# Kernel optimization log

Measured on AMD Instinct MI355X. Metric: run time of the kernel, lower is better.

The kernel has to match this reference:

```python
import jax, jax.numpy as jnp
import numpy as np

N = 100000     # nodes
H = 128        # hidden_channels == in_channels
OUT = 64       # out_channels
L = 3          # num_layers=4 -> num_layers-1 Layer modules
E = 1_600_000  # unique undirected edges (avg degree 16)
BN_EPS = 1e-5


def _make_edges():
    # Unique undirected edges, no self-loops -> dense symmetric adjacency in the
    # original module is exactly this edge set symmetrized.
    rng = np.random.default_rng(0)
    i = rng.integers(0, N, 1_700_000)
    j = rng.integers(0, N, 1_700_000)
    m = i != j
    i, j = i[m], j[m]
    lo, hi = np.minimum(i, j), np.maximum(i, j)
    pairs = np.unique(lo.astype(np.int64) * N + hi)[:E]
    lo = (pairs // N).astype(np.int32)
    hi = (pairs % N).astype(np.int32)
    src = jnp.asarray(np.concatenate([lo, hi]))  # [2E] directed
    dst = jnp.asarray(np.concatenate([hi, lo]))
    return src, dst


def setup_inputs() -> dict:
    key = jax.random.key(0)
    ks = jax.random.split(key, 24)
    nrm = lambda k, s: (jax.random.normal(k, s, dtype=jnp.float32) * 0.05)
    src, dst = _make_edges()
    return {
        "x": jax.random.normal(ks[0], (N, H), dtype=jnp.float32),
        "src": src,
        "dst": dst,
        # per-Layer MLP(in=H, hidden=H, out=H): Linear->ReLU->Linear, stacked over L
        "layer_W1": nrm(ks[1], (L, H, H)),
        "layer_b1": nrm(ks[2], (L, H)),
        "layer_W2": nrm(ks[3], (L, H, H)),
        "layer_b2": nrm(ks[4], (L, H)),
        # BatchNorm1d (eval mode: running stats)
        "bn_gamma": 1.0 + nrm(ks[5], (L, H)),
        "bn_beta": nrm(ks[6], (L, H)),
        "bn_mean": nrm(ks[7], (L, H)),
        "bn_var": jax.random.uniform(ks[8], (L, H), jnp.float32, 0.5, 1.5),
        # single shared GRUCell(H, H)
        "gru_Wih": nrm(ks[9], (3 * H, H)),
        "gru_Whh": nrm(ks[10], (3 * H, H)),
        "gru_bih": nrm(ks[11], (3 * H,)),
        "gru_bhh": nrm(ks[12], (3 * H,)),
        # mlp_last: MLP(H, H, OUT)
        "last_W1": nrm(ks[13], (H, H)),
        "last_b1": nrm(ks[14], (H,)),
        "last_W2": nrm(ks[15], (OUT, H)),
        "last_b2": nrm(ks[16], (OUT,)),
    }


def reference(x, src, dst, layer_W1, layer_b1, layer_W2, layer_b2,
              bn_gamma, bn_beta, bn_mean, bn_var,
              gru_Wih, gru_Whh, gru_bih, gru_bhh,
              last_W1, last_b1, last_W2, last_b2):
    n = x.shape[0]
    deg = jax.ops.segment_sum(jnp.ones(src.shape[0], x.dtype), dst, num_segments=n)
    inv_deg = (1.0 / jnp.maximum(deg, 1.0))[:, None]  # isolated nodes -> 0 agg
    h = jnp.zeros((n, H), x.dtype)
    for l in range(L):
        agg = jax.ops.segment_sum(x[src], dst, num_segments=n) * inv_deg  # mean over neighbors
        c = x + agg
        c = jnp.maximum(c @ layer_W1[l].T + layer_b1[l], 0.0) @ layer_W2[l].T + layer_b2[l]
        c = bn_gamma[l] * (c - bn_mean[l]) * jax.lax.rsqrt(bn_var[l] + BN_EPS) + bn_beta[l]
        # F.dropout(training=False) is identity
        gi = c @ gru_Wih.T + gru_bih  # [n, 3H]
        gh = h @ gru_Whh.T + gru_bhh
        r = jax.nn.sigmoid(gi[:, :H] + gh[:, :H])
        z = jax.nn.sigmoid(gi[:, H:2 * H] + gh[:, H:2 * H])
        nst = jnp.tanh(gi[:, 2 * H:] + r * gh[:, 2 * H:])
        h = (1.0 - z) * nst + z * h
        x = h
    return jnp.maximum(x @ last_W1.T + last_b1, 0.0) @ last_W2.T + last_b2
```

## Files before the change

### kernel.cpp

```cpp
#include <hip/hip_runtime.h>
#include <hip/hip_bf16.h>
#include <stdint.h>

typedef __bf16 bf16;
typedef __bf16 bf16x8 __attribute__((ext_vector_type(8)));
typedef float f32x4 __attribute__((ext_vector_type(4)));
typedef float f32x2 __attribute__((ext_vector_type(2)));
typedef uint32_t u32x4 __attribute__((ext_vector_type(4)));

#define HD 128
#define LDP (HD + 8)
#define NTPB 4
#define MFMA __builtin_amdgcn_mfma_f32_16x16x32_bf16

__device__ inline float bflo(uint32_t u){ return __uint_as_float(u << 16); }
__device__ inline float bfhi(uint32_t u){ return __uint_as_float(u & 0xffff0000u); }
__device__ inline uint32_t packbf(float a, float b){
    bf16 x = (bf16)a, y = (bf16)b;
    uint16_t ux = __builtin_bit_cast(uint16_t, x), uy = __builtin_bit_cast(uint16_t, y);
    return (uint32_t)ux | ((uint32_t)uy << 16);
}
__device__ inline bf16x8 ldb8(const bf16* p){ return *(const bf16x8*)p; }
__device__ inline float sigm(float x){ return 1.f / (1.f + __expf(-x)); }
__device__ inline float tanh_fast(float x){ float t = __expf(-2.f * x); return (1.f - t) / (1.f + t); }
__device__ inline uint32_t swz(uint32_t b){ return b ^ (((b >> 8) & 7u) << 4); }

__global__ void k_cvt(const float* __restrict__ in, bf16* __restrict__ out, int n){
    int i = blockIdx.x * 256 + threadIdx.x;
    if (i < n) out[i] = (bf16)in[i];
}

__global__ void k_cvt_x(const float* __restrict__ in, uint32_t* __restrict__ out, int nU){
    int i = blockIdx.x * 256 + threadIdx.x;
    if (i >= nU) return;
    int r = i >> 6, dw = i & 63;
    uint32_t v = packbf(in[(size_t)i * 2], in[(size_t)i * 2 + 1]);
    int slot = dw >> 2, w = dw & 3;
    out[(size_t)r * 64 + (((slot ^ (r & 7)) << 2) | w)] = v;
}

__global__ void k_bound(const int* __restrict__ dstB, int E, int* __restrict__ rows2, int n){
    int v = blockIdx.x * 256 + threadIdx.x;
    if (v > n) return;
    int lo = 0, hi = E;
    while (lo < hi){ int mid = (lo + hi) >> 1; if (dstB[mid] < v) lo = mid + 1; else hi = mid; }
    rows2[v] = lo;
}

__global__ void k_count(const int* __restrict__ dst, int* __restrict__ deg, int ne){
    int i = blockIdx.x * 256 + threadIdx.x;
    if (i < ne) atomicAdd(&deg[dst[i]], 1);
}

__global__ void k_scan1(const int* __restrict__ deg, int* __restrict__ rows,
                        int* __restrict__ bsum, int n){
    __shared__ int lds[256];
    int b = blockIdx.x, tid = threadIdx.x;
    int i0 = b * 1024 + tid * 4;
    int v[4]; int s = 0;
#pragma unroll
    for (int j = 0; j < 4; ++j){ int idx = i0 + j; v[j] = (idx < n) ? deg[idx] : 0; s += v[j]; }
    lds[tid] = s; __syncthreads();
    int acc = s;
    for (int off = 1; off < 256; off <<= 1){
        int add = (tid >= off) ? lds[tid - off] : 0;
        __syncthreads();
        acc += add; lds[tid] = acc;
        __syncthreads();
    }
    int run = acc - s;
#pragma unroll
    for (int j = 0; j < 4; ++j){ int idx = i0 + j; if (idx < n) rows[idx] = run; run += v[j]; }
    if (tid == 255) bsum[b] = acc;
}

__global__ void k_scan2(int* __restrict__ bsum, int nb){
    __shared__ int lds[128];
    int tid = threadIdx.x;
    int v = (tid < nb) ? bsum[tid] : 0;
    lds[tid] = v; __syncthreads();
    int acc = v;
    for (int off = 1; off < 128; off <<= 1){
        int add = (tid >= off) ? lds[tid - off] : 0;
        __syncthreads();
        acc += add; lds[tid] = acc;
        __syncthreads();
    }
    if (tid < nb) bsum[tid] = acc - v;
}

__global__ void k_scan3(int* __restrict__ rows, const int* __restrict__ bsum, int n, int total){
    int i = blockIdx.x * 256 + threadIdx.x;
    if (i < n) rows[i] += bsum[i >> 10];
    if (i == n) rows[n] = total;
}

__global__ void k_fillp(const int* __restrict__ src, const int* __restrict__ dst,
                        int* __restrict__ cur, int* __restrict__ col, int ne, int nPerG){
    int g = blockIdx.x & 7;
    int i = (blockIdx.x >> 3) * 256 + threadIdx.x;
    if (i >= ne) return;
    int d = dst[i];
    int lo = g * nPerG;
    if (d >= lo && d < lo + nPerG){
        int p = atomicAdd(&cur[d], 1);
        col[p] = src[i];
    }
}

__global__ __launch_bounds__(256) void k_gather(
    const bf16* __restrict__ curx,
    const int* __restrict__ srcB, const int* __restrict__ rows2,
    const int* __restrict__ colB, const int* __restrict__ rowsB,
    bf16* __restrict__ cout, int n)
{
    int wid = threadIdx.x >> 6, lane = threadIdx.x & 63;
    int v = blockIdx.x * 4 + wid;
    if (v >= n) return;
    int grp = lane >> 3, sl = lane & 7;
    int a0 = rows2[v], a1 = rows2[v + 1];
    int b0 = rowsB[v], b1 = rowsB[v + 1];
    int deg = (a1 - a0) + (b1 - b0);
    float inv = (deg > 0) ? 1.f / (float)deg : 0.f;

    const u32x4* base = (const u32x4*)curx;
    f32x2 acc2[8];
#pragma unroll
    for (int k = 0; k < 8; ++k) acc2[k] = (f32x2){0.f, 0.f};

    for (int j = a0 + grp; j < a1; j += 8){
        int nb = srcB[j];
        int px = nb & 7;
        u32x4 q0 = base[(size_t)nb * 16 + (sl ^ px)];
        u32x4 q1 = base[(size_t)nb * 16 + 8 + (sl ^ px)];
#pragma unroll
        for (int k = 0; k < 4; ++k){
            acc2[k]     += (f32x2){bflo(q0[k]), bfhi(q0[k])};
            acc2[4 + k] += (f32x2){bflo(q1[k]), bfhi(q1[k])};
        }
    }
    for (int j = b0 + grp; j < b1; j += 8){
        int nb = colB[j];
        int px = nb & 7;
        u32x4 q0 = base[(size_t)nb * 16 + (sl ^ px)];
        u32x4 q1 = base[(size_t)nb * 16 + 8 + (sl ^ px)];
#pragma unroll
        for (int k = 0; k < 4; ++k){
            acc2[k]     += (f32x2){bflo(q0[k]), bfhi(q0[k])};
            acc2[4 + k] += (f32x2){bflo(q1[k]), bfhi(q1[k])};
        }
    }
    float acc[16];
#pragma unroll
    for (int k = 0; k < 4; ++k){
        acc[2*k]     = acc2[k].x;     acc[2*k+1]     = acc2[k].y;
        acc[8+2*k]   = acc2[4+k].x;   acc[8+2*k+1]   = acc2[4+k].y;
    }
#pragma unroll
    for (int k = 0; k < 16; ++k){
        acc[k] += __shfl_xor(acc[k], 8);
        acc[k] += __shfl_xor(acc[k], 16);
        acc[k] += __shfl_xor(acc[k], 32);
    }
    if (grp == 0){
        int pv = v & 7;
        u32x4 x0 = base[(size_t)v * 16 + (sl ^ pv)];
        u32x4 x1 = base[(size_t)v * 16 + 8 + (sl ^ pv)];
        u32x4 o0, o1;
#pragma unroll
        for (int k = 0; k < 4; ++k){
            o0[k] = packbf(bflo(x0[k]) + acc[2*k] * inv,   bfhi(x0[k]) + acc[2*k+1] * inv);
            o1[k] = packbf(bflo(x1[k]) + acc[8+2*k] * inv, bfhi(x1[k]) + acc[8+2*k+1] * inv);
        }
        ((u32x4*)cout)[(size_t)v * 16 + (sl ^ pv)]     = o0;
        ((u32x4*)cout)[(size_t)v * 16 + 8 + (sl ^ pv)] = o1;
    }
}

#define CL0 0u
#define CL1 32768u
#define HL0 65536u
#define ALO 98304u
__global__ __launch_bounds__(512, 1) void k_layer(
    const bf16* __restrict__ cin, const bf16* __restrict__ hOld, bf16* __restrict__ hNew,
    const bf16* __restrict__ W1, const float* __restrict__ b1,
    const bf16* __restrict__ W2, const float* __restrict__ b2,
    const float* __restrict__ gm, const float* __restrict__ bt,
    const float* __restrict__ mu, const float* __restrict__ vr,
    const bf16* __restrict__ Wih, const bf16* __restrict__ Whh,
    const float* __restrict__ bih, const float* __restrict__ bhh, int nT)
{
    __shared__ __align__(16) char smem[131072];
    int tid = threadIdx.x, wid = tid >> 6, lane = tid & 63;
    int rA = lane & 15, u = lane >> 4, ko = u * 8;
    int c = wid * 16 + rA;

    bf16x8 W1f[4], W2f[4], Gri[4], Grh[4], Gzi[4], Gzh[4], Gni[4], Gnh[4];
#pragma unroll
    for (int kk = 0; kk < 4; ++kk){
        W1f[kk] = ldb8(W1  + (size_t)c * HD + ko + kk * 32);
        W2f[kk] = ldb8(W2  + (size_t)c * HD + ko + kk * 32);
        Gri[kk] = ldb8(Wih + (size_t)c * HD + ko + kk * 32);
        Gzi[kk] = ldb8(Wih + (size_t)(c + 128) * HD + ko + kk * 32);
        Gni[kk] = ldb8(Wih + (size_t)(c + 256) * HD + ko + kk * 32);
        Grh[kk] = ldb8(Whh + (size_t)c * HD + ko + kk * 32);
        Gzh[kk] = ldb8(Whh + (size_t)(c + 128) * HD + ko + kk * 32);
        Gnh[kk] = ldb8(Whh + (size_t)(c + 256) * HD + ko + kk * 32);
    }
    float b1c = b1[c];
    float bnS = gm[c] * rsqrtf(vr[c] + 1e-5f);
    float bnO = bt[c] - mu[c] * bnS;
    float b2c = b2[c];
    float br = bih[c] + bhh[c], bz = bih[c + 128] + bhh[c + 128];
    float bin = bih[c + 256], bhn = bhh[c + 256];

    auto gload = [&](const char* g, uint32_t lo){
        __builtin_amdgcn_global_load_lds(
            (const __attribute__((address_space(1))) void*)g,
            (__attribute__((address_space(3))) void*)(smem + lo), 16, 0, 0);
    };
    auto stageC = [&](int t, uint32_t dst){
        const char* g = (const char*)cin + (size_t)t * 32768 + (size_t)lane * 16;
#pragma unroll
        for (int i = 0; i < 4; ++i){
            uint32_t ch = (uint32_t)(wid * 4 + i) * 1024;
            gload(g + ch, dst + ch);
        }
    };
    auto stageH = [&](int t){
        const char* g = (const char*)hOld + (size_t)t * 32768 + (size_t)lane * 16;
#pragma unroll
        for (int i = 0; i < 4; ++i){
            uint32_t ch = (uint32_t)(wid * 4 + i) * 1024;
            gload(g + ch, HL0 + ch);
        }
    };

    int t = blockIdx.x;
    int cur = 0;
    if (t < nT) stageC(t, CL0);
    for (; t < nT; t += (int)gridDim.x){
        __syncthreads();
        stageH(t);
        int tn = t + (int)gridDim.x;
        if (tn < nT) stageC(tn, cur ? CL0 : CL1);
        uint32_t CB = cur ? CL1 : CL0;

#pragma unroll
        for (int m = 0; m < 8; ++m){
            bf16x8 a_[4];
#pragma unroll
            for (int kk = 0; kk < 4; ++kk){
                uint32_t b = (uint32_t)(m * 16 + rA) * 256 + (uint32_t)(u * 16 + kk * 64);
                a_[kk] = *(const bf16x8*)(smem + CB + swz(b));
            }
            f32x4 acc = {0,0,0,0};
#pragma unroll
            for (int kk = 0; kk < 4; ++kk) acc = MFMA(a_[kk], W1f[kk], acc, 0, 0, 0);
#pragma unroll
            for (int j = 0; j < 4; ++j){
                uint32_t r = (uint32_t)(m * 16 + u * 4 + j);
                *(bf16*)(smem + ALO + swz(r * 256 + (uint32_t)c * 2)) =
                    (bf16)fmaxf(acc[j] + b1c, 0.f);
            }
        }
        asm volatile("s_waitcnt lgkmcnt(0)" ::: "memory");
        __builtin_amdgcn_sched_barrier(0);
        __builtin_amdgcn_s_barrier();

#pragma unroll
        for (int m = 0; m < 8; ++m){
            bf16x8 a_[4];
#pragma unroll
            for (int kk = 0; kk < 4; ++kk){
                uint32_t b = (uint32_t)(m * 16 + rA) * 256 + (uint32_t)(u * 16 + kk * 64);
                a_[kk] = *(const bf16x8*)(smem + ALO + swz(b));
            }
            f32x4 acc = {0,0,0,0};
#pragma unroll
            for (int kk = 0; kk < 4; ++kk) acc = MFMA(a_[kk], W2f[kk], acc, 0, 0, 0);
#pragma unroll
            for (int j = 0; j < 4; ++j){
                uint32_t r = (uint32_t)(m * 16 + u * 4 + j);
                *(bf16*)(smem + CB + swz(r * 256 + (uint32_t)c * 2)) =
                    (bf16)((acc[j] + b2c) * bnS + bnO);
            }
        }
        if (tn < nT){ asm volatile("s_waitcnt vmcnt(4) lgkmcnt(0)" ::: "memory"); }
        else        { asm volatile("s_waitcnt vmcnt(0) lgkmcnt(0)" ::: "memory"); }
        __builtin_amdgcn_sched_barrier(0);
        __builtin_amdgcn_s_barrier();

#pragma unroll
        for (int m = 0; m < 8; ++m){
            bf16x8 ac_[4], ah_[4];
#pragma unroll
            for (int kk = 0; kk < 4; ++kk){
                uint32_t b = (uint32_t)(m * 16 + rA) * 256 + (uint32_t)(u * 16 + kk * 64);
                ac_[kk] = *(const bf16x8*)(smem + CB + swz(b));
                ah_[kk] = *(const bf16x8*)(smem + HL0 + swz(b));
            }
            f32x4 rr = {0,0,0,0}, zz = {0,0,0,0}, gi = {0,0,0,0}, gh = {0,0,0,0};
#pragma unroll
            for (int kk = 0; kk < 4; ++kk){
                rr = MFMA(ac_[kk], Gri[kk], rr, 0, 0, 0);
                rr = MFMA(ah_[kk], Grh[kk], rr, 0, 0, 0);
                zz = MFMA(ac_[kk], Gzi[kk], zz, 0, 0, 0);
                zz = MFMA(ah_[kk], Gzh[kk], zz, 0, 0, 0);
                gi = MFMA(ac_[kk], Gni[kk], gi, 0, 0, 0);
                gh = MFMA(ah_[kk], Gnh[kk], gh, 0, 0, 0);
            }
#pragma unroll
            for (int j = 0; j < 4; ++j){
                uint32_t r = (uint32_t)(m * 16 + u * 4 + j);
                uint32_t inner = swz(r * 256 + (uint32_t)c * 2);
                float hold = (float)*(const bf16*)(smem + HL0 + inner);
                float rg = sigm(rr[j] + br);
                float zg = sigm(zz[j] + bz);
                float ng = tanh_fast(gi[j] + bin + rg * (gh[j] + bhn));
                *(bf16*)(smem + ALO + inner) = (bf16)((1.f - zg) * ng + zg * hold);
            }
        }
        asm volatile("s_waitcnt lgkmcnt(0)" ::: "memory");
        __builtin_amdgcn_sched_barrier(0);
        __builtin_amdgcn_s_barrier();

        {
            char* hNb = (char*)hNew + (size_t)t * 32768;
#pragma unroll
            for (int i = 0; i < 4; ++i){
                uint32_t off = (uint32_t)tid * 16 + (uint32_t)i * 8192;
                *(u32x4*)(hNb + off) = *(const u32x4*)(smem + ALO + off);
            }
        }
        cur ^= 1;
    }
}

__global__ __launch_bounds__(256) void k_final(
    const bf16* __restrict__ hin, const bf16* __restrict__ W1, const float* __restrict__ b1,
    const bf16* __restrict__ W2, const float* __restrict__ b2,
    float* __restrict__ out, int nTiles)
{
    __shared__ bf16 lds[NTPB][16][LDP];
    int wid = threadIdx.x >> 6, lane = threadIdx.x & 63;
    int tile = blockIdx.x * NTPB + wid;
    if (tile >= nTiles) return;
    int r0 = tile * 16;
    int rA = lane & 15, u = lane >> 4, ko = u * 8;

    bf16x8 a[4];
    const char* hb = (const char*)hin;
    uint32_t b0 = (uint32_t)(r0 + rA) * 256 + (uint32_t)(u * 16);
#pragma unroll
    for (int kk = 0; kk < 4; ++kk) a[kk] = *(const bf16x8*)(hb + swz(b0 + (uint32_t)kk * 64));

#pragma unroll
    for (int t = 0; t < 8; ++t){
        f32x4 acc = {0.f, 0.f, 0.f, 0.f};
        int c = t * 16 + rA;
        const bf16* bp = W1 + (size_t)c * HD + ko;
#pragma unroll
        for (int kk = 0; kk < 4; ++kk)
            acc = MFMA(a[kk], ldb8(bp + kk * 32), acc, 0, 0, 0);
        float bias = b1[c];
#pragma unroll
        for (int j = 0; j < 4; ++j){
            float v = fmaxf(acc[j] + bias, 0.f);
            lds[wid][u * 4 + j][c] = (bf16)v;
        }
    }
    __threadfence_block();
    bf16x8 a2[4];
    const bf16* lp = &lds[wid][rA][ko];
#pragma unroll
    for (int kk = 0; kk < 4; ++kk) a2[kk] = ldb8(lp + kk * 32);

#pragma unroll
    for (int t = 0; t < 4; ++t){
        f32x4 acc = {0.f, 0.f, 0.f, 0.f};
        int c = t * 16 + rA;
        const bf16* bp = W2 + (size_t)c * HD + ko;
#pragma unroll
        for (int kk = 0; kk < 4; ++kk)
            acc = MFMA(a2[kk], ldb8(bp + kk * 32), acc, 0, 0, 0);
        float bias = b2[c];
#pragma unroll
        for (int j = 0; j < 4; ++j)
            out[(size_t)(r0 + u * 4 + j) * 64 + c] = acc[j] + bias;
    }
}

extern "C" void kernel_launch(void* const* d_in, const int* in_sizes, int n_in,
                              void* d_out, int out_size, void* d_ws, size_t ws_size,
                              hipStream_t stream)
{
    const float* x    = (const float*)d_in[0];
    const int*   src  = (const int*)d_in[1];
    const int*   dst  = (const int*)d_in[2];
    const float* lW1  = (const float*)d_in[3];
    const float* lb1  = (const float*)d_in[4];
    const float* lW2  = (const float*)d_in[5];
    const float* lb2  = (const float*)d_in[6];
    const float* gmm  = (const float*)d_in[7];
    const float* bta  = (const float*)d_in[8];
    const float* mun  = (const float*)d_in[9];
    const float* vrr  = (const float*)d_in[10];
    const float* Wih  = (const float*)d_in[11];
    const float* Whh  = (const float*)d_in[12];
    const float* bih  = (const float*)d_in[13];
    const float* bhh  = (const float*)d_in[14];
    const float* fW1  = (const float*)d_in[15];
    const float* fb1  = (const float*)d_in[16];
    const float* fW2  = (const float*)d_in[17];
    const float* fb2  = (const float*)d_in[18];

    int n  = in_sizes[0] / HD;
    int ne = in_sizes[1];
    int E  = ne / 2;
    int L  = in_sizes[3] / (HD * HD);
    int nPad = (n + 127) & ~127;

    char* w = (char*)d_ws;
    auto alloc = [&](size_t bytes) -> char* {
        char* p = w; w += (bytes + 255) & ~(size_t)255; return p;
    };
    bf16* xbf  = (bf16*)alloc((size_t)nPad * HD * 2);
    bf16* hA   = (bf16*)alloc((size_t)nPad * HD * 2);
    bf16* hB   = (bf16*)alloc((size_t)nPad * HD * 2);
    bf16* cin  = (bf16*)alloc((size_t)nPad * HD * 2);
    bf16* W1b  = (bf16*)alloc((size_t)L * HD * HD * 2);
    bf16* W2b  = (bf16*)alloc((size_t)L * HD * HD * 2);
    bf16* Wib  = (bf16*)alloc((size_t)3 * HD * HD * 2);
    bf16* Whb  = (bf16*)alloc((size_t)3 * HD * HD * 2);
    bf16* fW1b = (bf16*)alloc((size_t)HD * HD * 2);
    bf16* fW2b = (bf16*)alloc((size_t)64 * HD * 2);
    int*  degB = (int*)alloc((size_t)n * 4);
    int*  rowsB= (int*)alloc((size_t)(n + 1) * 4);
    int*  rows2= (int*)alloc((size_t)(n + 1) * 4);
    int*  bsum = (int*)alloc(512);
    int*  curB = (int*)alloc((size_t)n * 4);
    int*  colB = (int*)alloc((size_t)E * 4);

    auto cvt = [&](const float* i, bf16* o, int cnt){
        k_cvt<<<(cnt + 255) / 256, 256, 0, stream>>>(i, o, cnt);
    };
    int nU = n * 64;
    k_cvt_x<<<(nU + 255) / 256, 256, 0, stream>>>(x, (uint32_t*)xbf, nU);
    cvt(lW1, W1b,  L * HD * HD);
    cvt(lW2, W2b,  L * HD * HD);
    cvt(Wih, Wib,  3 * HD * HD);
    cvt(Whh, Whb,  3 * HD * HD);
    cvt(fW1, fW1b, HD * HD);
    cvt(fW2, fW2b, 64 * HD);

    hipMemsetAsync(degB, 0, (size_t)n * 4, stream);
    hipMemsetAsync(hA, 0, (size_t)nPad * HD * 2, stream);

    k_bound<<<(n + 1 + 255) / 256, 256, 0, stream>>>(dst + E, E, rows2, n);
    k_count<<<(E + 255) / 256, 256, 0, stream>>>(dst, degB, E);
    int nb = (n + 1023) / 1024;
    k_scan1<<<nb, 256, 0, stream>>>(degB, rowsB, bsum, n);
    k_scan2<<<1, 128, 0, stream>>>(bsum, nb);
    k_scan3<<<(n + 1 + 255) / 256, 256, 0, stream>>>(rowsB, bsum, n, E);
    hipMemcpyAsync(curB, rowsB, (size_t)n * 4, hipMemcpyDeviceToDevice, stream);
    int nPerG = (n + 7) / 8;
    k_fillp<<<8 * ((E + 255) / 256), 256, 0, stream>>>(src, dst, curB, colB, E, nPerG);

    int nT128 = nPad / 128;
    int nT16 = (n + 15) / 16;
    int gF = (nT16 + NTPB - 1) / NTPB;

    const bf16* curp = xbf;
    for (int l = 0; l < L; ++l){
        k_gather<<<(n + 3) / 4, 256, 0, stream>>>(curp, src + E, rows2, colB, rowsB, cin, n);
        k_layer<<<256, 512, 0, stream>>>(cin, hA, hB,
            W1b + (size_t)l * HD * HD, lb1 + l * HD,
            W2b + (size_t)l * HD * HD, lb2 + l * HD,
            gmm + l * HD, bta + l * HD, mun + l * HD, vrr + l * HD,
            Wib, Whb, bih, bhh, nT128);
        bf16* tmp = hA; hA = hB; hB = tmp;
        curp = hA;
    }
    k_final<<<gF, 256, 0, stream>>>(hA, fW1b, fb1, fW2b, fb2, (float*)d_out, nT16);
}
```

Before: 761.7 us.

## Split fused layer kernel into separate MLP and GRU kernels with double-buffered staging

The fused per-layer kernel is split in two. k_mlp runs the MLP and BatchNorm on 64-row tiles with 48KB of LDS and launch bounds allowing 4 blocks per CU, then writes the normalized activations to a new global buffer. k_gru runs on 96-row tiles and double-buffers both the c and h inputs, so the next tile's loads overlap the current tile's compute. This cuts register and LDS pressure per kernel and improves load overlap. The cost is an extra global round trip of the N×128 bf16 activations and one more launch per layer.

```diff
diff --git a/kernel.cpp b/kernel.cpp
--- a/kernel.cpp
+++ b/kernel.cpp
@@ -177,29 +177,135 @@
     }
 }
 
-#define CL0 0u
-#define CL1 32768u
-#define HL0 65536u
-#define ALO 98304u
-__global__ __launch_bounds__(512, 1) void k_layer(
-    const bf16* __restrict__ cin, const bf16* __restrict__ hOld, bf16* __restrict__ hNew,
+#define MT_C0 0u
+#define MT_C1 16384u
+#define MT_A  32768u
+__global__ __launch_bounds__(512, 4) void k_mlp(
+    const bf16* __restrict__ cin, bf16* __restrict__ cbn,
     const bf16* __restrict__ W1, const float* __restrict__ b1,
     const bf16* __restrict__ W2, const float* __restrict__ b2,
     const float* __restrict__ gm, const float* __restrict__ bt,
-    const float* __restrict__ mu, const float* __restrict__ vr,
+    const float* __restrict__ mu, const float* __restrict__ vr, int nT)
+{
+    __shared__ __align__(16) char smem[49152];
+    int tid = threadIdx.x, wid = tid >> 6, lane = tid & 63;
+    int rA = lane & 15, u = lane >> 4, ko = u * 8;
+    int c = wid * 16 + rA;
+
+    bf16x8 W1f[4], W2f[4];
+#pragma unroll
+    for (int kk = 0; kk < 4; ++kk){
+        W1f[kk] = ldb8(W1 + (size_t)c * HD + ko + kk * 32);
+        W2f[kk] = ldb8(W2 + (size_t)c * HD + ko + kk * 32);
+    }
+    float b1c = b1[c];
+    float bnS = gm[c] * rsqrtf(vr[c] + 1e-5f);
+    float bnO = bt[c] - mu[c] * bnS;
+    float b2c = b2[c];
+
+    auto gload = [&](const char* g, uint32_t lo){
+        __builtin_amdgcn_global_load_lds(
+            (const __attribute__((address_space(1))) void*)g,
+            (__attribute__((address_space(3))) void*)(smem + lo), 16, 0, 0);
+    };
+    auto stageC = [&](int t, uint32_t dst){
+        const char* g = (const char*)cin + (size_t)t * 16384 + (size_t)lane * 16;
+#pragma unroll
+        for (int i = 0; i < 2; ++i){
+            uint32_t ch = (uint32_t)(wid * 2 + i) * 1024;
+            gload(g + ch, dst + ch);
+        }
+    };
+
+    int t = blockIdx.x;
+    int cur = 0;
+    if (t < nT) stageC(t, MT_C0);
+    asm volatile("s_waitcnt vmcnt(0) lgkmcnt(0)" ::: "memory");
+    __builtin_amdgcn_sched_barrier(0);
+    __builtin_amdgcn_s_barrier();
+
+    for (; t < nT; t += (int)gridDim.x){
+        int tn = t + (int)gridDim.x;
+        if (tn < nT) stageC(tn, cur ? MT_C0 : MT_C1);
+        uint32_t CB = cur ? MT_C1 : MT_C0;
+
+#pragma unroll
+        for (int m = 0; m < 4; ++m){
+            bf16x8 a_[4];
+#pragma unroll
+            for (int kk = 0; kk < 4; ++kk){
+                uint32_t b = (uint32_t)(m * 16 + rA) * 256 + (uint32_t)(u * 16 + kk * 64);
+                a_[kk] = *(const bf16x8*)(smem + CB + swz(b));
+            }
+            f32x4 acc = {0,0,0,0};
+#pragma unroll
+            for (int kk = 0; kk < 4; ++kk) acc = MFMA(a_[kk], W1f[kk], acc, 0, 0, 0);
+#pragma unroll
+            for (int j = 0; j < 4; ++j){
+                uint32_t r = (uint32_t)(m * 16 + u * 4 + j);
+                *(bf16*)(smem + MT_A + swz(r * 256 + (uint32_t)c * 2)) =
+                    (bf16)fmaxf(acc[j] + b1c, 0.f);
+            }
+        }
+        asm volatile("s_waitcnt lgkmcnt(0)" ::: "memory");
+        __builtin_amdgcn_sched_barrier(0);
+        __builtin_amdgcn_s_barrier();
+
+#pragma unroll
+        for (int m = 0; m < 4; ++m){
+            bf16x8 a_[4];
+#pragma unroll
+            for (int kk = 0; kk < 4; ++kk){
+                uint32_t b = (uint32_t)(m * 16 + rA) * 256 + (uint32_t)(u * 16 + kk * 64);
+                a_[kk] = *(const bf16x8*)(smem + MT_A + swz(b));
+            }
+            f32x4 acc = {0,0,0,0};
+#pragma unroll
+            for (int kk = 0; kk < 4; ++kk) acc = MFMA(a_[kk], W2f[kk], acc, 0, 0, 0);
+#pragma unroll
+            for (int j = 0; j < 4; ++j){
+                uint32_t r = (uint32_t)(m * 16 + u * 4 + j);
+                *(bf16*)(smem + CB + swz(r * 256 + (uint32_t)c * 2)) =
+                    (bf16)((acc[j] + b2c) * bnS + bnO);
+            }
+        }
+        asm volatile("s_waitcnt lgkmcnt(0)" ::: "memory");
+        __builtin_amdgcn_sched_barrier(0);
+        __builtin_amdgcn_s_barrier();
+
+        {
+            char* gout = (char*)cbn + (size_t)t * 16384;
+#pragma unroll
+            for (int i = 0; i < 2; ++i){
+                uint32_t off = (uint32_t)tid * 16 + (uint32_t)i * 8192;
+                *(u32x4*)(gout + off) = *(const u32x4*)(smem + CB + off);
+            }
+        }
+        asm volatile("s_waitcnt vmcnt(2) lgkmcnt(0)" ::: "memory");
+        __builtin_amdgcn_sched_barrier(0);
+        __builtin_amdgcn_s_barrier();
+        cur ^= 1;
+    }
+}
+
+#define GT_C0 0u
+#define GT_C1 24576u
+#define GT_H0 49152u
+#define GT_H1 73728u
+#define GT_O  98304u
+__global__ __launch_bounds__(512, 1) void k_gru(
+    const bf16* __restrict__ cbn, const bf16* __restrict__ hOld, bf16* __restrict__ hNew,
     const bf16* __restrict__ Wih, const bf16* __restrict__ Whh,
     const float* __restrict__ bih, const float* __restrict__ bhh, int nT)
 {
-    __shared__ __align__(16) char smem[131072];
+    __shared__ __align__(16) char smem[122880];
     int tid = threadIdx.x, wid = tid >> 6, lane = tid & 63;
     int rA = lane & 15, u = lane >> 4, ko = u * 8;
     int c = wid * 16 + rA;
 
-    bf16x8 W1f[4], W2f[4], Gri[4], Grh[4], Gzi[4], Gzh[4], Gni[4], Gnh[4];
+    bf16x8 Gri[4], Grh[4], Gzi[4], Gzh[4], Gni[4], Gnh[4];
 #pragma unroll
     for (int kk = 0; kk < 4; ++kk){
-        W1f[kk] = ldb8(W1  + (size_t)c * HD + ko + kk * 32);
-        W2f[kk] = ldb8(W2  + (size_t)c * HD + ko + kk * 32);
         Gri[kk] = ldb8(Wih + (size_t)c * HD + ko + kk * 32);
         Gzi[kk] = ldb8(Wih + (size_t)(c + 128) * HD + ko + kk * 32);
         Gni[kk] = ldb8(Wih + (size_t)(c + 256) * HD + ko + kk * 32);
@@ -207,10 +313,6 @@
         Gzh[kk] = ldb8(Whh + (size_t)(c + 128) * HD + ko + kk * 32);
         Gnh[kk] = ldb8(Whh + (size_t)(c + 256) * HD + ko + kk * 32);
     }
-    float b1c = b1[c];
-    float bnS = gm[c] * rsqrtf(vr[c] + 1e-5f);
-    float bnO = bt[c] - mu[c] * bnS;
-    float b2c = b2[c];
     float br = bih[c] + bhh[c], bz = bih[c + 128] + bhh[c + 128];
     float bin = bih[c + 256], bhn = bhh[c + 256];
 
@@ -220,85 +322,46 @@
             (__attribute__((address_space(3))) void*)(smem + lo), 16, 0, 0);
     };
     auto stageC = [&](int t, uint32_t dst){
-        const char* g = (const char*)cin + (size_t)t * 32768 + (size_t)lane * 16;
-#pragma unroll
-        for (int i = 0; i < 4; ++i){
-            uint32_t ch = (uint32_t)(wid * 4 + i) * 1024;
+        const char* g = (const char*)cbn + (size_t)t * 24576 + (size_t)lane * 16;
+#pragma unroll
+        for (int i = 0; i < 3; ++i){
+            uint32_t ch = (uint32_t)(wid * 3 + i) * 1024;
             gload(g + ch, dst + ch);
         }
     };
-    auto stageH = [&](int t){
-        const char* g = (const char*)hOld + (size_t)t * 32768 + (size_t)lane * 16;
-#pragma unroll
-        for (int i = 0; i < 4; ++i){
-            uint32_t ch = (uint32_t)(wid * 4 + i) * 1024;
-            gload(g + ch, HL0 + ch);
+    auto stageH = [&](int t, uint32_t dst){
+        const char* g = (const char*)hOld + (size_t)t * 24576 + (size_t)lane * 16;
+#pragma unroll
+        for (int i = 0; i < 3; ++i){
+            uint32_t ch = (uint32_t)(wid * 3 + i) * 1024;
+            gload(g + ch, dst + ch);
         }
     };
 
     int t = blockIdx.x;
     int cur = 0;
-    if (t < nT) stageC(t, CL0);
+    if (t < nT){ stageC(t, GT_C0); stageH(t, GT_H0); }
+    asm volatile("s_waitcnt vmcnt(0) lgkmcnt(0)" ::: "memory");
+    __builtin_amdgcn_sched_barrier(0);
+    __builtin_amdgcn_s_barrier();
+
     for (; t < nT; t += (int)gridDim.x){
-        __syncthreads();
-        stageH(t);
         int tn = t + (int)gridDim.x;
-        if (tn < nT) stageC(tn, cur ? CL0 : CL1);
-        uint32_t CB = cur ? CL1 : CL0;
-
-#pragma unroll
-        for (int m = 0; m < 8; ++m){
-            bf16x8 a_[4];
-#pragma unroll
-            for (int kk = 0; kk < 4; ++kk){
-                uint32_t b = (uint32_t)(m * 16 + rA) * 256 + (uint32_t)(u * 16 + kk * 64);
-                a_[kk] = *(const bf16x8*)(smem + CB + swz(b));
-            }
-            f32x4 acc = {0,0,0,0};
-#pragma unroll
-            for (int kk = 0; kk < 4; ++kk) acc = MFMA(a_[kk], W1f[kk], acc, 0, 0, 0);
-#pragma unroll
-            for (int j = 0; j < 4; ++j){
-                uint32_t r = (uint32_t)(m * 16 + u * 4 + j);
-                *(bf16*)(smem + ALO + swz(r * 256 + (uint32_t)c * 2)) =
-                    (bf16)fmaxf(acc[j] + b1c, 0.f);
-            }
-        }
-        asm volatile("s_waitcnt lgkmcnt(0)" ::: "memory");
-        __builtin_amdgcn_sched_barrier(0);
-        __builtin_amdgcn_s_barrier();
-
-#pragma unroll
-        for (int m = 0; m < 8; ++m){
-            bf16x8 a_[4];
-#pragma unroll
-            for (int kk = 0; kk < 4; ++kk){
-                uint32_t b = (uint32_t)(m * 16 + rA) * 256 + (uint32_t)(u * 16 + kk * 64);
-                a_[kk] = *(const bf16x8*)(smem + ALO + swz(b));
-            }
-            f32x4 acc = {0,0,0,0};
-#pragma unroll
-            for (int kk = 0; kk < 4; ++kk) acc = MFMA(a_[kk], W2f[kk], acc, 0, 0, 0);
-#pragma unroll
-            for (int j = 0; j < 4; ++j){
-                uint32_t r = (uint32_t)(m * 16 + u * 4 + j);
-                *(bf16*)(smem + CB + swz(r * 256 + (uint32_t)c * 2)) =
-                    (bf16)((acc[j] + b2c) * bnS + bnO);
-            }
-        }
-        if (tn < nT){ asm volatile("s_waitcnt vmcnt(4) lgkmcnt(0)" ::: "memory"); }
-        else        { asm volatile("s_waitcnt vmcnt(0) lgkmcnt(0)" ::: "memory"); }
-        __builtin_amdgcn_sched_barrier(0);
-        __builtin_amdgcn_s_barrier();
-
-#pragma unroll
-        for (int m = 0; m < 8; ++m){
+        if (tn < nT){
+            stageC(tn, cur ? GT_C0 : GT_C1);
+            stageH(tn, cur ? GT_H0 : GT_H1);
+        }
+        uint32_t CB = cur ? GT_C1 : GT_C0;
+        uint32_t HB = cur ? GT_H1 : GT_H0;
+
+#pragma unroll
+        for (int m = 0; m < 6; ++m){
             bf16x8 ac_[4], ah_[4];
 #pragma unroll
             for (int kk = 0; kk < 4; ++kk){
                 uint32_t b = (uint32_t)(m * 16 + rA) * 256 + (uint32_t)(u * 16 + kk * 64);
                 ac_[kk] = *(const bf16x8*)(smem + CB + swz(b));
-                ah_[kk] = *(const bf16x8*)(smem + HL0 + swz(b));
+                ah_[kk] = *(const bf16x8*)(smem + HB + swz(b));
             }
             f32x4 rr = {0,0,0,0}, zz = {0,0,0,0}, gi = {0,0,0,0}, gh = {0,0,0,0};
 #pragma unroll
@@ -314,11 +377,11 @@
             for (int j = 0; j < 4; ++j){
                 uint32_t r = (uint32_t)(m * 16 + u * 4 + j);
                 uint32_t inner = swz(r * 256 + (uint32_t)c * 2);
-                float hold = (float)*(const bf16*)(smem + HL0 + inner);
+                float hold = (float)*(const bf16*)(smem + HB + inner);
                 float rg = sigm(rr[j] + br);
                 float zg = sigm(zz[j] + bz);
                 float ng = tanh_fast(gi[j] + bin + rg * (gh[j] + bhn));
-                *(bf16*)(smem + ALO + inner) = (bf16)((1.f - zg) * ng + zg * hold);
+                *(bf16*)(smem + GT_O + inner) = (bf16)((1.f - zg) * ng + zg * hold);
             }
         }
         asm volatile("s_waitcnt lgkmcnt(0)" ::: "memory");
@@ -326,13 +389,16 @@
         __builtin_amdgcn_s_barrier();
 
         {
-            char* hNb = (char*)hNew + (size_t)t * 32768;
-#pragma unroll
-            for (int i = 0; i < 4; ++i){
+            char* hNb = (char*)hNew + (size_t)t * 24576;
+#pragma unroll
+            for (int i = 0; i < 3; ++i){
                 uint32_t off = (uint32_t)tid * 16 + (uint32_t)i * 8192;
-                *(u32x4*)(hNb + off) = *(const u32x4*)(smem + ALO + off);
-            }
-        }
+                *(u32x4*)(hNb + off) = *(const u32x4*)(smem + GT_O + off);
+            }
+        }
+        asm volatile("s_waitcnt vmcnt(3) lgkmcnt(0)" ::: "memory");
+        __builtin_amdgcn_sched_barrier(0);
+        __builtin_amdgcn_s_barrier();
         cur ^= 1;
     }
 }
@@ -419,7 +485,7 @@
     int ne = in_sizes[1];
     int E  = ne / 2;
     int L  = in_sizes[3] / (HD * HD);
-    int nPad = (n + 127) & ~127;
+    int nPad = (n + 191) / 192 * 192;
 
     char* w = (char*)d_ws;
     auto alloc = [&](size_t bytes) -> char* {
@@ -429,6 +495,7 @@
     bf16* hA   = (bf16*)alloc((size_t)nPad * HD * 2);
     bf16* hB   = (bf16*)alloc((size_t)nPad * HD * 2);
     bf16* cin  = (bf16*)alloc((size_t)nPad * HD * 2);
+    bf16* cbn  = (bf16*)alloc((size_t)nPad * HD * 2);
     bf16* W1b  = (bf16*)alloc((size_t)L * HD * HD * 2);
     bf16* W2b  = (bf16*)alloc((size_t)L * HD * HD * 2);
     bf16* Wib  = (bf16*)alloc((size_t)3 * HD * HD * 2);
@@ -467,18 +534,21 @@
     int nPerG = (n + 7) / 8;
     k_fillp<<<8 * ((E + 255) / 256), 256, 0, stream>>>(src, dst, curB, colB, E, nPerG);
 
-    int nT128 = nPad / 128;
+    int nT64 = nPad / 64;
+    int nT96 = nPad / 96;
+    int gM = (nT64 < 512) ? nT64 : 512;
+    int gG = (nT96 < 256) ? nT96 : 256;
     int nT16 = (n + 15) / 16;
     int gF = (nT16 + NTPB - 1) / NTPB;
 
     const bf16* curp = xbf;
     for (int l = 0; l < L; ++l){
         k_gather<<<(n + 3) / 4, 256, 0, stream>>>(curp, src + E, rows2, colB, rowsB, cin, n);
-        k_layer<<<256, 512, 0, stream>>>(cin, hA, hB,
+        k_mlp<<<gM, 512, 0, stream>>>(cin, cbn,
             W1b + (size_t)l * HD * HD, lb1 + l * HD,
             W2b + (size_t)l * HD * HD, lb2 + l * HD,
-            gmm + l * HD, bta + l * HD, mun + l * HD, vrr + l * HD,
-            Wib, Whb, bih, bhh, nT128);
+            gmm + l * HD, bta + l * HD, mun + l * HD, vrr + l * HD, nT64);
+        k_gru<<<gG, 512, 0, stream>>>(cbn, hA, hB, Wib, Whb, bih, bhh, nT96);
         bf16* tmp = hA; hA = hB; hB = tmp;
         curp = hA;
     }
```

Result: no change. 748.0 us (-1.8%).
